# Kernel tuning notes

Hardware: AMD Instinct MI355X
Metric: run time of the kernel (lower is better)

Reference implementation:

```python
import jax, jax.numpy as jnp
import numpy as np

N = 128
HID = 512
NUM_IRREPS = 7

_ISO = np.array([
    [1,0,1,0,0,0,0],
    [0,1,0,1,1,0,0],
    [1,0,1,0,0,0,0],
    [0,1,0,1,1,0,0],
    [0,1,0,1,1,0,0],
    [0,0,0,0,0,1,0],
    [0,0,0,0,0,0,1],
], dtype=np.float32)


def setup_inputs() -> dict:
    key = jax.random.key(0)
    k1, k2 = jax.random.split(key)
    x = jax.random.normal(k1, (2, N, N, HID), dtype=jnp.float32)
    # xavier_uniform with relu gain on [num_irreps, num_irreps]
    gain = float(np.sqrt(2.0))
    bound = gain * float(np.sqrt(6.0 / (NUM_IRREPS + NUM_IRREPS)))
    weight = jax.random.uniform(k2, (NUM_IRREPS, NUM_IRREPS), dtype=jnp.float32,
                                minval=-bound, maxval=bound)
    iso_matrix = jnp.asarray(_ISO)
    return {"x": x, "weight": weight, "iso_matrix": iso_matrix}


def _decompose(M):
    # M: [h, n, n] -> [7, h, n, n], isotypic components under S_n conjugation.
    n = M.shape[-1]
    eye = jnp.eye(n, dtype=M.dtype)
    off = 1.0 - eye
    d = jnp.diagonal(M, axis1=-2, axis2=-1)                 # [h, n]
    dbar = jnp.mean(d, axis=-1, keepdims=True)              # [h, 1]
    P1 = dbar[..., None] * eye                              # diag mean (trivial)
    P2 = (d - dbar)[..., None] * eye                        # diag deviation (standard)
    O = M * off                                             # off-diagonal part
    s = jnp.sum(O, axis=(-2, -1)) / (n * (n - 1))           # [h]
    P3 = s[..., None, None] * off                           # offdiag mean (trivial)
    Op = O - P3
    r = jnp.sum(Op, axis=-1)                                # row sums, [h, n]
    c = jnp.sum(Op, axis=-2)                                # col sums, [h, n]
    xr = ((n - 1) * r + c) / (n * (n - 2))
    yc = ((n - 1) * c + r) / (n * (n - 2))
    P4 = xr[..., :, None] * off                             # row standard copy
    P5 = yc[..., None, :] * off                             # col standard copy
    R = Op - P4 - P5                                        # zero diag / row / col sums
    Rt = jnp.swapaxes(R, -1, -2)
    P6 = 0.5 * (R + Rt)                                     # irrep (n-2,2)
    P7 = 0.5 * (R - Rt)                                     # irrep (n-2,1,1)
    return jnp.stack([P1, P2, P3, P4, P5, P6, P7])          # [7, h, n, n]


def reference(x, weight, iso_matrix):
    # x: [2, n, n, hidden] -> transpose(1,3): [2, hidden, n, n]
    xt = jnp.transpose(x, (0, 3, 2, 1))
    A, B = xt[0], xt[1]                                     # [h, n, n]
    params = weight * iso_matrix                            # [7, 7]
    a = _decompose(A)                                       # [7, h, n, n]
    b = _decompose(B)
    # params @ comps, then sum over output irrep axis (fused into one einsum)
    A_out = jnp.einsum('ij,jhmn->hmn', params, a)
    B_out = jnp.einsum('ij,jhmn->hmn', params, b)
    out = jnp.stack([A_out, B_out])                         # [2, h, n, n]
    return jnp.transpose(out, (0, 3, 2, 1))                 # [2, n, n, hidden]
```

## Files before the change

### kernel.cpp

```cpp
#include <hip/hip_runtime.h>
#include <math.h>

#define N 128
#define HID 512
#define NH (N * HID)
#define SNH ((size_t)N * NH)
#define NPAIRS (N * (N + 1) / 2)

typedef float vf4 __attribute__((ext_vector_type(4)));
union F4 { vf4 v; float f[4]; };
typedef unsigned int u32t;
typedef unsigned short u16t;

__device__ __forceinline__ u32t pk2(float a, float b) {
    u32t ua = __float_as_uint(a), ub = __float_as_uint(b);
    ua = (ua + 0x7FFFu + ((ua >> 16) & 1u)) >> 16;
    ub = (ub + 0x7FFFu + ((ub >> 16) & 1u)) >> 16;
    return ua | (ub << 16);
}
__device__ __forceinline__ void stbf4(u16t* p, F4 t) {
    uint2 u; u.x = pk2(t.f[0], t.f[1]); u.y = pk2(t.f[2], t.f[3]);
    *reinterpret_cast<uint2*>(p) = u;
}
__device__ __forceinline__ F4 ldbf4(const u16t* p) {
    const uint2 u = *reinterpret_cast<const uint2*>(p);
    F4 r;
    r.f[0] = __uint_as_float(u.x << 16);
    r.f[1] = __uint_as_float(u.x & 0xFFFF0000u);
    r.f[2] = __uint_as_float(u.y << 16);
    r.f[3] = __uint_as_float(u.y & 0xFFFF0000u);
    return r;
}

__global__ __launch_bounds__(512)
void schur_p1(const float* __restrict__ x, u16t* __restrict__ PScol,
              u16t* __restrict__ PSrow, float* __restrict__ Dg) {
    const int u  = blockIdx.x;
    const int hq = u & 3;
    const int bq = (u >> 2) & 3;
    const int g  = (u >> 4) & 7;
    const int s  = u >> 7;
    const int tid = threadIdx.x;
    const int f   = tid & 31;
    const int bg  = tid >> 5;
    const int b0  = bq * 32 + bg * 2;
    const int hoff = hq * 128 + f * 4;

    const float* xs   = x + (size_t)s * SNH;
    const float* base = xs + (size_t)(g * 16) * NH + b0 * HID + hoff;

    __shared__ F4 rowred[8][16][32];

    F4 acc0, acc1;
    acc0.v = (vf4)(0.f); acc1.v = (vf4)(0.f);

    #pragma unroll
    for (int c = 0; c < 2; ++c) {
        #pragma unroll
        for (int al = 0; al < 8; ++al) {
            const float* p = base + (size_t)(c * 8 + al) * NH;
            F4 v0; v0.v = *reinterpret_cast<const vf4*>(p);
            F4 v1; v1.v = *reinterpret_cast<const vf4*>(p + HID);
            acc0.v += v0.v;
            acc1.v += v1.v;
            F4 rs; rs.v = v0.v + v1.v;
            rowred[al][bg][f] = rs;
        }
        __syncthreads();
        if (tid < 256) {
            const int ar = tid >> 5;
            const int f2 = tid & 31;
            F4 t; t.v = (vf4)(0.f);
            #pragma unroll
            for (int k = 0; k < 16; ++k) t.v += rowred[ar][k][f2].v;
            const int a = g * 16 + c * 8 + ar;
            stbf4(PSrow + ((((size_t)s * 4 + bq) * N + a) * HID + hq * 128 + f2 * 4), t);
        }
        __syncthreads();
    }

    stbf4(PScol + ((((size_t)s * 8 + g) * N + b0) * HID + hoff), acc0);
    stbf4(PScol + ((((size_t)s * 8 + g) * N + b0 + 1) * HID + hoff), acc1);

    if (bq == (g >> 1)) {
        const int ar = tid >> 5;
        const int f2 = tid & 31;
        const int a  = g * 16 + ar;
        const vf4 dv = *reinterpret_cast<const vf4*>(
            xs + (size_t)a * NH + a * HID + hq * 128 + f2 * 4);
        *reinterpret_cast<vf4*>(Dg +
            (((size_t)s * N + a) * HID + hq * 128 + f2 * 4)) = dv;
    }
}

__global__ __launch_bounds__(256)
void schur_p2(const u16t* __restrict__ PScol, const u16t* __restrict__ PSrow,
              const float* __restrict__ Dg,
              u16t* __restrict__ Xr, u16t* __restrict__ Yc,
              float* __restrict__ Sv, float* __restrict__ Db) {
    const int bi = blockIdx.x;
    const int s  = bi >> 4;
    const int hc = bi & 15;
    const int tid = threadIdx.x;
    const int iq = tid >> 3;
    const int hf = tid & 7;
    const int h  = (hc * 8 + hf) * 4;

    F4 sa[4], sb[4], dg[4];
    F4 T, D; T.v = (vf4)(0.f); D.v = (vf4)(0.f);
    #pragma unroll
    for (int k = 0; k < 4; ++k) {
        const int i = iq + 32 * k;
        F4 acc; acc.v = (vf4)(0.f);
        #pragma unroll
        for (int gg = 0; gg < 8; ++gg)
            acc.v += ldbf4(PScol + (((size_t)s * 8 + gg) * N + i) * HID + h).v;
        sa[k] = acc; T.v += acc.v;
        F4 accb; accb.v = (vf4)(0.f);
        #pragma unroll
        for (int qq = 0; qq < 4; ++qq)
            accb.v += ldbf4(PSrow + (((size_t)s * 4 + qq) * N + i) * HID + h).v;
        sb[k] = accb;
        dg[k].v = *reinterpret_cast<const vf4*>(Dg + ((size_t)s * N + i) * HID + h);
        D.v += dg[k].v;
    }

    __shared__ F4 redT[32][8];
    __shared__ F4 redD[32][8];
    __shared__ F4 shS[8];
    redT[iq][hf] = T;
    redD[iq][hf] = D;
    __syncthreads();
    if (iq == 0) {
        F4 Tt, Dd; Tt.v = (vf4)(0.f); Dd.v = (vf4)(0.f);
        #pragma unroll
        for (int q = 0; q < 32; ++q) { Tt.v += redT[q][hf].v; Dd.v += redD[q][hf].v; }
        F4 sh, db_;
        sh.v  = (Tt.v - Dd.v) * (1.0f / 16256.0f);
        db_.v = Dd.v * (1.0f / 128.0f);
        *reinterpret_cast<vf4*>(Sv + s * HID + h) = sh.v;
        *reinterpret_cast<vf4*>(Db + s * HID + h) = db_.v;
        shS[hf] = sh;
    }
    __syncthreads();

    const F4 sh = shS[hf];
    const float inv = 1.0f / 16128.0f;
    const size_t base = (size_t)s * N * HID;
    #pragma unroll
    for (int k = 0; k < 4; ++k) {
        const int i = iq + 32 * k;
        F4 r, c, xr, yc;
        r.v = sa[k].v - dg[k].v - 127.0f * sh.v;
        c.v = sb[k].v - dg[k].v - 127.0f * sh.v;
        xr.v = (127.0f * r.v + c.v) * inv;
        yc.v = (127.0f * c.v + r.v) * inv;
        stbf4(Xr + base + (size_t)i * HID + h, xr);
        stbf4(Yc + base + (size_t)i * HID + h, yc);
    }
}

__global__ __launch_bounds__(256)
void schur_p3(const float* __restrict__ x, const float* __restrict__ w,
              const float* __restrict__ iso,
              const u16t* __restrict__ Xr, const u16t* __restrict__ Yc,
              const float* __restrict__ Sv, const float* __restrict__ Db,
              float* __restrict__ out) {
    const int t  = threadIdx.x;
    const int k  = t >> 7;
    const int ht = t & 127;
    const int hoff = ht * 4;

    float c[7];
    #pragma unroll
    for (int j = 0; j < 7; ++j) {
        float acc = 0.f;
        #pragma unroll
        for (int i = 0; i < 7; ++i) acc += w[i * 7 + j] * iso[i * 7 + j];
        c[j] = acc;
    }
    const float c1 = c[0], c2 = c[1], c3 = c[2], c4 = c[3], c5 = c[4];
    const float al = 0.5f * (c[5] + c[6]);
    const float be = 0.5f * (c[5] - c[6]);

    const int bid = blockIdx.x;
    const int swz = (bid & 7) * 258 + (bid >> 3);
    const int pg0 = swz * 8;

    #define TRI_OFF(aa) ((aa) * N - (((aa) * ((aa) - 1)) >> 1))
    #pragma unroll
    for (int it = 0; it < 4; ++it) {
        const int pg = pg0 + it * 2 + k;
        const int s  = (pg >= NPAIRS) ? 1 : 0;
        const int p  = pg - s * NPAIRS;

        int a = (int)((257.0f - sqrtf((float)(66049 - 8 * p))) * 0.5f);
        if (a < 0) a = 0;
        if (a > N - 1) a = N - 1;
        while (a > 0 && TRI_OFF(a) > p) --a;
        while (TRI_OFF(a + 1) <= p) ++a;
        const int b = a + (p - TRI_OFF(a));

        const size_t sbase    = (size_t)s * SNH;
        const size_t statbase = (size_t)s * N * HID;

        if (a == b) {
            F4 v;  v.v  = *reinterpret_cast<const vf4*>(x + sbase + ((size_t)a * N + a) * HID + hoff);
            F4 db; db.v = *reinterpret_cast<const vf4*>(Db + (size_t)s * HID + hoff);
            F4 o;
            #pragma unroll
            for (int j = 0; j < 4; ++j)
                o.f[j] = c1 * db.f[j] + c2 * (v.f[j] - db.f[j]);
            __builtin_nontemporal_store(o.v,
                reinterpret_cast<vf4*>(out + sbase + ((size_t)a * N + a) * HID + hoff));
            continue;
        }

        F4 va;  va.v  = *reinterpret_cast<const vf4*>(x + sbase + ((size_t)a * N + b) * HID + hoff);
        F4 vb;  vb.v  = *reinterpret_cast<const vf4*>(x + sbase + ((size_t)b * N + a) * HID + hoff);
        F4 xra = ldbf4(Xr + statbase + (size_t)a * HID + hoff);
        F4 xrb = ldbf4(Xr + statbase + (size_t)b * HID + hoff);
        F4 yca = ldbf4(Yc + statbase + (size_t)a * HID + hoff);
        F4 ycb = ldbf4(Yc + statbase + (size_t)b * HID + hoff);
        F4 sh;  sh.v  = *reinterpret_cast<const vf4*>(Sv + (size_t)s * HID + hoff);

        F4 oab, oba;
        #pragma unroll
        for (int j = 0; j < 4; ++j) {
            const float U = va.f[j] - sh.f[j] - xrb.f[j] - yca.f[j];
            const float V = vb.f[j] - sh.f[j] - xra.f[j] - ycb.f[j];
            oab.f[j] = c3 * sh.f[j] + c4 * xrb.f[j] + c5 * yca.f[j] + al * U + be * V;
            oba.f[j] = c3 * sh.f[j] + c4 * xra.f[j] + c5 * ycb.f[j] + al * V + be * U;
        }
        __builtin_nontemporal_store(oab.v,
            reinterpret_cast<vf4*>(out + sbase + ((size_t)a * N + b) * HID + hoff));
        __builtin_nontemporal_store(oba.v,
            reinterpret_cast<vf4*>(out + sbase + ((size_t)b * N + a) * HID + hoff));
    }
}

extern "C" void kernel_launch(void* const* d_in, const int* in_sizes, int n_in,
                              void* d_out, int out_size, void* d_ws, size_t ws_size,
                              hipStream_t stream) {
    const float* x   = (const float*)d_in[0];
    const float* w   = (const float*)d_in[1];
    const float* iso = (const float*)d_in[2];
    float* out = (float*)d_out;
    char* wsb  = (char*)d_ws;

    u16t*  PScol = (u16t*)(wsb);
    u16t*  PSrow = (u16t*)(wsb + (4u << 20));
    float* Dg    = (float*)(wsb + (8u << 20));
    u16t*  Xr    = (u16t*)(wsb + (12u << 20));
    u16t*  Yc    = (u16t*)(wsb + (14u << 20));
    float* Sv    = (float*)(wsb + (16u << 20));
    float* Db    = (float*)(wsb + (16u << 20) + 65536);

    schur_p1<<<256, 512, 0, stream>>>(x, PScol, PSrow, Dg);
    schur_p2<<<32, 256, 0, stream>>>(PScol, PSrow, Dg, Xr, Yc, Sv, Db);
    schur_p3<<<2064, 256, 0, stream>>>(x, w, iso, Xr, Yc, Sv, Db, out);
}
```

Baseline: 45.06 us.

## Tile phase-3 over 8x8 (a,b) blocks to reuse per-row stats

The final elementwise kernel now gives each 512-thread block one upper-triangular 8x8 tile of (a,b) pairs per sample. It loads the bf16 row/col statistics for the 8 b-rows once into registers and reuses them across the a-rows, replacing per-pair triangular index solving and redundant stat loads. The grid shrinks from 2064 to 272 blocks, which reduces parallelism and raises register pressure (16 F4 arrays held live). Diagonal tiles do extra branching to skip the lower triangle.

Result: slower. 51.96 us (+15.3%).

```diff
diff --git a/kernel.cpp b/kernel.cpp
--- a/kernel.cpp
+++ b/kernel.cpp
@@ -160,16 +160,16 @@
     }
 }
 
-__global__ __launch_bounds__(256)
+__global__ __launch_bounds__(512)
 void schur_p3(const float* __restrict__ x, const float* __restrict__ w,
               const float* __restrict__ iso,
               const u16t* __restrict__ Xr, const u16t* __restrict__ Yc,
               const float* __restrict__ Sv, const float* __restrict__ Db,
               float* __restrict__ out) {
-    const int t  = threadIdx.x;
-    const int k  = t >> 7;
-    const int ht = t & 127;
-    const int hoff = ht * 4;
+    const int tid = threadIdx.x;
+    const int f   = tid & 127;
+    const int q   = tid >> 7;
+    const int hoff = f * 4;
 
     float c[7];
     #pragma unroll
@@ -184,58 +184,72 @@
     const float be = 0.5f * (c[5] - c[6]);
 
     const int bid = blockIdx.x;
-    const int swz = (bid & 7) * 258 + (bid >> 3);
-    const int pg0 = swz * 8;
-
-    #define TRI_OFF(aa) ((aa) * N - (((aa) * ((aa) - 1)) >> 1))
-    #pragma unroll
-    for (int it = 0; it < 4; ++it) {
-        const int pg = pg0 + it * 2 + k;
-        const int s  = (pg >= NPAIRS) ? 1 : 0;
-        const int p  = pg - s * NPAIRS;
-
-        int a = (int)((257.0f - sqrtf((float)(66049 - 8 * p))) * 0.5f);
-        if (a < 0) a = 0;
-        if (a > N - 1) a = N - 1;
-        while (a > 0 && TRI_OFF(a) > p) --a;
-        while (TRI_OFF(a + 1) <= p) ++a;
-        const int b = a + (p - TRI_OFF(a));
-
-        const size_t sbase    = (size_t)s * SNH;
-        const size_t statbase = (size_t)s * N * HID;
-
-        if (a == b) {
-            F4 v;  v.v  = *reinterpret_cast<const vf4*>(x + sbase + ((size_t)a * N + a) * HID + hoff);
-            F4 db; db.v = *reinterpret_cast<const vf4*>(Db + (size_t)s * HID + hoff);
-            F4 o;
+    const int swz = (bid & 7) * 34 + (bid >> 3);
+    const int s   = (swz >= 136) ? 1 : 0;
+    const int tp  = swz - s * 136;
+
+    #define OFF16(r) ((r) * 16 - (((r) * ((r) - 1)) >> 1))
+    int ar = 0;
+    while (OFF16(ar + 1) <= tp) ++ar;
+    const int br = ar + (tp - OFF16(ar));
+    const bool diag = (ar == br);
+
+    const size_t sbase    = (size_t)s * SNH;
+    const size_t statbase = (size_t)s * N * HID;
+
+    F4 sh; sh.v = *reinterpret_cast<const vf4*>(Sv + (size_t)s * HID + hoff);
+    F4 db; db.v = *reinterpret_cast<const vf4*>(Db + (size_t)s * HID + hoff);
+
+    F4 xrb[8], ycb[8];
+    #pragma unroll
+    for (int bl = 0; bl < 8; ++bl) {
+        const int gb = br * 8 + bl;
+        xrb[bl] = ldbf4(Xr + statbase + (size_t)gb * HID + hoff);
+        ycb[bl] = ldbf4(Yc + statbase + (size_t)gb * HID + hoff);
+    }
+
+    #pragma unroll
+    for (int aq = 0; aq < 2; ++aq) {
+        const int alc = q * 2 + aq;
+        const int ga  = ar * 8 + alc;
+        const F4 xra = ldbf4(Xr + statbase + (size_t)ga * HID + hoff);
+        const F4 yca = ldbf4(Yc + statbase + (size_t)ga * HID + hoff);
+        const float* rowA = x   + sbase + (size_t)ga * NH + hoff;
+        float*       orwA = out + sbase + (size_t)ga * NH + hoff;
+
+        #pragma unroll
+        for (int bl = 0; bl < 8; ++bl) {
+            const int gb = br * 8 + bl;
+            if (diag) {
+                if (bl < alc) continue;
+                if (bl == alc) {
+                    F4 v; v.v = *reinterpret_cast<const vf4*>(rowA + gb * HID);
+                    F4 o;
+                    #pragma unroll
+                    for (int j = 0; j < 4; ++j)
+                        o.f[j] = c1 * db.f[j] + c2 * (v.f[j] - db.f[j]);
+                    __builtin_nontemporal_store(o.v,
+                        reinterpret_cast<vf4*>(orwA + gb * HID));
+                    continue;
+                }
+            }
+            F4 va; va.v = *reinterpret_cast<const vf4*>(rowA + gb * HID);
+            F4 vb; vb.v = *reinterpret_cast<const vf4*>(
+                x + sbase + (size_t)gb * NH + ga * HID + hoff);
+
+            F4 oab, oba;
             #pragma unroll
-            for (int j = 0; j < 4; ++j)
-                o.f[j] = c1 * db.f[j] + c2 * (v.f[j] - db.f[j]);
-            __builtin_nontemporal_store(o.v,
-                reinterpret_cast<vf4*>(out + sbase + ((size_t)a * N + a) * HID + hoff));
-            continue;
+            for (int j = 0; j < 4; ++j) {
+                const float U = va.f[j] - sh.f[j] - xrb[bl].f[j] - yca.f[j];
+                const float V = vb.f[j] - sh.f[j] - xra.f[j] - ycb[bl].f[j];
+                oab.f[j] = c3 * sh.f[j] + c4 * xrb[bl].f[j] + c5 * yca.f[j] + al * U + be * V;
+                oba.f[j] = c3 * sh.f[j] + c4 * xra.f[j] + c5 * ycb[bl].f[j] + al * V + be * U;
+            }
+            __builtin_nontemporal_store(oab.v,
+                reinterpret_cast<vf4*>(orwA + gb * HID));
+            __builtin_nontemporal_store(oba.v,
+                reinterpret_cast<vf4*>(out + sbase + (size_t)gb * NH + ga * HID + hoff));
         }
-
-        F4 va;  va.v  = *reinterpret_cast<const vf4*>(x + sbase + ((size_t)a * N + b) * HID + hoff);
-        F4 vb;  vb.v  = *reinterpret_cast<const vf4*>(x + sbase + ((size_t)b * N + a) * HID + hoff);
-        F4 xra = ldbf4(Xr + statbase + (size_t)a * HID + hoff);
-        F4 xrb = ldbf4(Xr + statbase + (size_t)b * HID + hoff);
-        F4 yca = ldbf4(Yc + statbase + (size_t)a * HID + hoff);
-        F4 ycb = ldbf4(Yc + statbase + (size_t)b * HID + hoff);
-        F4 sh;  sh.v  = *reinterpret_cast<const vf4*>(Sv + (size_t)s * HID + hoff);
-
-        F4 oab, oba;
-        #pragma unroll
-        for (int j = 0; j < 4; ++j) {
-            const float U = va.f[j] - sh.f[j] - xrb.f[j] - yca.f[j];
-            const float V = vb.f[j] - sh.f[j] - xra.f[j] - ycb.f[j];
-            oab.f[j] = c3 * sh.f[j] + c4 * xrb.f[j] + c5 * yca.f[j] + al * U + be * V;
-            oba.f[j] = c3 * sh.f[j] + c4 * xra.f[j] + c5 * ycb.f[j] + al * V + be * U;
-        }
-        __builtin_nontemporal_store(oab.v,
-            reinterpret_cast<vf4*>(out + sbase + ((size_t)a * N + b) * HID + hoff));
-        __builtin_nontemporal_store(oba.v,
-            reinterpret_cast<vf4*>(out + sbase + ((size_t)b * N + a) * HID + hoff));
     }
 }
 
@@ -258,5 +272,5 @@
 
     schur_p1<<<256, 512, 0, stream>>>(x, PScol, PSrow, Dg);
     schur_p2<<<32, 256, 0, stream>>>(PScol, PSrow, Dg, Xr, Yc, Sv, Db);
-    schur_p3<<<2064, 256, 0, stream>>>(x, w, iso, Xr, Yc, Sv, Db, out);
-}
+    schur_p3<<<272, 512, 0, stream>>>(x, w, iso, Xr, Yc, Sv, Db, out);
+}
```
